# Kernel tuning notes

Measured on AMD Instinct MI355X. Metric: run time of the kernel, lower is better.

The kernel has to match this reference:

```python
import jax, jax.numpy as jnp
import numpy as np

N0, N1, N2 = 200000, 50000, 10000   # node counts per hop (src -> layer1 targets -> layer2 targets)
E1, E2 = 1000000, 250000
C_IN, H = 128, 256


def setup_inputs() -> dict:
    key = jax.random.key(0)
    ks = jax.random.split(key, 10)
    return {
        "x": jax.random.normal(ks[0], (N0, C_IN), dtype=jnp.float32),
        "src1": jax.random.randint(ks[1], (E1,), 0, N0, dtype=jnp.int32),
        "dst1": jax.random.randint(ks[2], (E1,), 0, N1, dtype=jnp.int32),
        "src2": jax.random.randint(ks[3], (E2,), 0, N1, dtype=jnp.int32),
        "dst2": jax.random.randint(ks[4], (E2,), 0, N2, dtype=jnp.int32),
        "Wl1": jax.random.normal(ks[5], (C_IN, H), dtype=jnp.float32) / np.sqrt(C_IN),
        "Wr1": jax.random.normal(ks[6], (C_IN, H), dtype=jnp.float32) / np.sqrt(C_IN),
        "b1": jnp.zeros((H,), dtype=jnp.float32),
        "Wl2": jax.random.normal(ks[7], (H, H), dtype=jnp.float32) / np.sqrt(H),
        "Wr2": jax.random.normal(ks[8], (H, H), dtype=jnp.float32) / np.sqrt(H),
        "b2": jnp.zeros((H,), dtype=jnp.float32),
    }


def _sage_conv(x_src, x_dst, src, dst, Wl, Wr, b, n_dst):
    # mean aggregation of neighbor messages (PyG SAGEConv, aggr='mean', root_weight=True)
    msgs = x_src[src]                                             # [E, C] irregular gather
    agg = jax.ops.segment_sum(msgs, dst, num_segments=n_dst)      # [n_dst, C]
    cnt = jax.ops.segment_sum(jnp.ones_like(dst, dtype=x_src.dtype), dst, num_segments=n_dst)
    agg = agg / jnp.maximum(cnt, 1.0)[:, None]
    return agg @ Wl + x_dst @ Wr + b


def reference(x, src1, dst1, src2, dst2, Wl1, Wr1, b1, Wl2, Wr2, b2):
    # layer 1: targets are first N1 nodes
    h = _sage_conv(x, x[:N1], src1, dst1, Wl1, Wr1, b1, N1)       # [N1, H]
    h = jax.nn.relu(h)                                            # dropout: eval mode (identity)
    # layer 2: targets are first N2 nodes of the layer-1 output
    out = _sage_conv(h, h[:N2], src2, dst2, Wl2, Wr2, b2, N2)     # [N2, H]
    return out
```

## Files before the change

kernel.cpp:

```cpp
#include <hip/hip_runtime.h>

#define N0 200000
#define N1 50000
#define N2 10000
#define E1 1000000
#define E2 250000
#define CIN 128
#define HD  256

#define SH1   6
#define PK1   18
#define NB1   782
#define CAP1  2048
#define DPB1  64
#define DPB1H 32
#define NB1L  1564
#define EB1H  1440
#define SH2   4
#define PK2   16
#define NB2   625
#define CAP2  640
#define DPB2  16

#define NBIN1 489
#define NBIN2 123
#define NPREP 768
#define NCVT  25000

#define EB2   (CAP2 + 128)

typedef __attribute__((ext_vector_type(8))) short short8;
typedef __attribute__((ext_vector_type(4))) float f32x4;
typedef __attribute__((ext_vector_type(2))) float f32x2;

__device__ __forceinline__ unsigned short f2bf(float f) {
    unsigned u = __builtin_bit_cast(unsigned, f);
    u = (u + 0x7fffu + ((u >> 16) & 1u)) >> 16;
    return (unsigned short)u;
}
__device__ __forceinline__ float bf2f(unsigned short h) {
    unsigned u = ((unsigned)h) << 16;
    return __builtin_bit_cast(float, u);
}

__device__ __forceinline__ unsigned enc_fp8x4(float a, float b, float c, float d) {
#if __has_builtin(__builtin_amdgcn_cvt_pk_fp8_f32)
    int p = 0;
    p = __builtin_amdgcn_cvt_pk_fp8_f32(a, b, p, false);
    p = __builtin_amdgcn_cvt_pk_fp8_f32(c, d, p, true);
    return (unsigned)p;
#else
    float vv[4] = {a, b, c, d};
    unsigned out = 0;
    #pragma unroll
    for (int k = 0; k < 4; k++) {
        float f = fminf(fmaxf(vv[k], -448.f), 448.f);
        unsigned u = __builtin_bit_cast(unsigned, f);
        const unsigned s = (u >> 24) & 0x80u;
        u &= 0x7fffffffu;
        unsigned byte;
        if (u < 0x3C800000u) {
            const float af = __builtin_bit_cast(float, u);
            byte = s | (unsigned)(int)rintf(af * 512.0f);
        } else {
            const unsigned u2 = u + 0x000FFFFFu + ((u >> 20) & 1u);
            const unsigned e  = (u2 >> 23) - 120u;
            byte = s | ((e & 0xFu) << 3) | ((u2 >> 20) & 7u);
        }
        out |= byte << (8 * k);
    }
    return out;
#endif
}

__device__ __forceinline__ unsigned char enc_fp8_1(float v) {
#if __has_builtin(__builtin_amdgcn_cvt_pk_fp8_f32)
    const int p = __builtin_amdgcn_cvt_pk_fp8_f32(v, v, 0, false);
    return (unsigned char)(p & 0xFF);
#else
    float f = fminf(fmaxf(v, -448.f), 448.f);
    unsigned u = __builtin_bit_cast(unsigned, f);
    const unsigned s = (u >> 24) & 0x80u;
    u &= 0x7fffffffu;
    unsigned byte;
    if (u < 0x3C800000u) {
        const float af = __builtin_bit_cast(float, u);
        byte = s | (unsigned)(int)rintf(af * 512.0f);
    } else {
        const unsigned u2 = u + 0x000FFFFFu + ((u >> 20) & 1u);
        const unsigned e  = (u2 >> 23) - 120u;
        byte = s | ((e & 0xFu) << 3) | ((u2 >> 20) & 7u);
    }
    return (unsigned char)byte;
#endif
}

__device__ __forceinline__ void acc_fp8x4(unsigned w, float* __restrict__ acc) {
#if __has_builtin(__builtin_amdgcn_cvt_pk_f32_fp8)
    const f32x2 lo = __builtin_amdgcn_cvt_pk_f32_fp8((int)w, false);
    const f32x2 hi = __builtin_amdgcn_cvt_pk_f32_fp8((int)w, true);
    acc[0] += lo[0]; acc[1] += lo[1]; acc[2] += hi[0]; acc[3] += hi[1];
#else
    #pragma unroll
    for (int k = 0; k < 4; k++) {
        const unsigned b8   = (w >> (8 * k)) & 0xFFu;
        const unsigned bits = ((b8 & 0x80u) << 24) | ((b8 & 0x7Fu) << 20);
        acc[k] += __builtin_bit_cast(float, bits) * 0x1p120f;
    }
#endif
}

template<int SHIFTB, int PACKSH, int CAP>
__device__ __forceinline__ void bin_body(
    int bb, const int* __restrict__ src, const int* __restrict__ dst,
    int* __restrict__ gcnt, unsigned* __restrict__ binned, int E, int* sh)
{
    int* hcnt  = sh;
    int* hbase = sh + 1024;
    int* hcur  = sh + 2048;
    const int t = threadIdx.x;
    #pragma unroll
    for (int j = 0; j < 4; j++) hcnt[t + j * 256] = 0;
    __syncthreads();

    unsigned pk[8];
    int      bk[8];
    const int e0 = bb * 2048;
    #pragma unroll
    for (int j = 0; j < 8; j++) {
        const int e = e0 + j * 256 + t;
        if (e < E) {
            const int d = dst[e];
            const int s = src[e];
            bk[j] = d >> SHIFTB;
            pk[j] = ((unsigned)(d & ((1 << SHIFTB) - 1)) << PACKSH) | (unsigned)s;
            atomicAdd(&hcnt[bk[j]], 1);
        } else bk[j] = -1;
    }
    __syncthreads();

    #pragma unroll
    for (int j = 0; j < 4; j++) {
        const int i = t + j * 256;
        hbase[i] = atomicAdd(&gcnt[i], hcnt[i]);
        hcur[i]  = 0;
    }
    __syncthreads();

    #pragma unroll
    for (int j = 0; j < 8; j++) {
        if (bk[j] >= 0) {
            const int idx = atomicAdd(&hcur[bk[j]], 1);
            binned[(size_t)bk[j] * CAP + hbase[bk[j]] + idx] = pk[j];
        }
    }
}

__global__ __launch_bounds__(256) void megaA_kernel(
    const float* __restrict__ x, unsigned short* __restrict__ xb,
    unsigned char* __restrict__ xf8, unsigned char* __restrict__ hb8,
    const float* __restrict__ Wl1, const float* __restrict__ Wr1,
    const float* __restrict__ Wl2, const float* __restrict__ Wr2,
    unsigned short* __restrict__ wsw1, unsigned short* __restrict__ wsw2,
    const int* __restrict__ src1, const int* __restrict__ dst1,
    const int* __restrict__ src2, const int* __restrict__ dst2,
    int* __restrict__ gcnt1, int* __restrict__ gcnt2,
    unsigned* __restrict__ binned1, unsigned* __restrict__ binned2)
{
    __shared__ int sh[3072];
    const int b = blockIdx.x;
    const int t = threadIdx.x;

    if (b < NBIN1) {
        bin_body<SH1, PK1, CAP1>(b, src1, dst1, gcnt1, binned1, E1, sh);
    } else if (b < NBIN1 + NBIN2) {
        bin_body<SH2, PK2, CAP2>(b - NBIN1, src2, dst2, gcnt2, binned2, E2, sh);
    } else if (b < NBIN1 + NBIN2 + NPREP) {
        const int pb = b - NBIN1 - NBIN2;
        const float* Wl; const float* Wr; unsigned short* wsw; int K, tid;
        if (pb < 256) { Wl = Wl1; Wr = Wr1; wsw = wsw1; K = CIN; tid = pb * 256 + t; }
        else          { Wl = Wl2; Wr = Wr2; wsw = wsw2; K = HD;  tid = (pb - 256) * 256 + t; }
        const int j  = tid & 7;
        const int L  = (tid >> 3) & 63;
        const int nt = (tid >> 9) & 15;
        const int kt = tid >> 13;
        const int k  = kt * 32 + (L >> 4) * 8 + j;
        const int n  = nt * 16 + (L & 15);
        const float v = (k < K) ? Wl[(size_t)k * HD + n]
                                : Wr[(size_t)(k - K) * HD + n];
        wsw[tid] = f2bf(v);
    } else if (b < NBIN1 + NBIN2 + NPREP + NCVT) {
        const int i = (b - NBIN1 - NBIN2 - NPREP) * 256 + t;
        const f32x4 v = __builtin_nontemporal_load(&((const f32x4*)x)[i]);
        ((unsigned*)xf8)[i] = enc_fp8x4(v.x, v.y, v.z, v.w);
        if (i < N1 * (CIN / 4)) {
            ushort4 o;
            o.x = f2bf(v.x); o.y = f2bf(v.y); o.z = f2bf(v.z); o.w = f2bf(v.w);
            ((ushort4*)xb)[i] = o;
        }
    } else {
        if (t < 32)  ((unsigned*)(xf8 + (size_t)N0 * CIN))[t] = 0u;
        if (t < 64)  ((unsigned*)(hb8 + (size_t)N1 * HD))[t] = 0u;
    }
}

__global__ __launch_bounds__(512) void layer1_mega(
    const unsigned short* __restrict__ xb, const unsigned char* __restrict__ xf8,
    const unsigned* __restrict__ binned1, const int* __restrict__ gcnt1,
    const unsigned short* __restrict__ wsw1, const float* __restrict__ bias,
    unsigned short* __restrict__ hb, unsigned char* __restrict__ hb8)
{
    __shared__ int ebuf[EB1H];
    __shared__ int lhist[DPB1H], loff[DPB1H], lcur[DPB1H];
    __shared__ __align__(16) unsigned short aggT[4 * DPB1H * 4 * 8];

    const int t = threadIdx.x;
    const int b = blockIdx.x;
    const int B = b >> 1;
    const int H = b & 1;
    const int cnt = gcnt1[B];
    const unsigned* bp = binned1 + (size_t)B * CAP1;

    if (t < DPB1H) lhist[t] = 0;
    __syncthreads();
    for (int i = t; i < cnt; i += 512) {
        const int r = (int)(bp[i] >> PK1) - H * DPB1H;
        if ((unsigned)r < (unsigned)DPB1H) atomicAdd(&lhist[r], 1);
    }
    __syncthreads();
    if (t < DPB1H) {
        const int p8 = (lhist[t] + 7) & ~7;
        int sum = p8;
        #pragma unroll
        for (int ofs = 1; ofs < DPB1H; ofs <<= 1) {
            const int u = __shfl_up(sum, ofs);
            if (t >= ofs) sum += u;
        }
        const int st = sum - p8;
        loff[t] = st; lcur[t] = st;
    }
    __syncthreads();
    for (int i = t; i < cnt; i += 512) {
        const unsigned p = bp[i];
        const int r = (int)(p >> PK1) - H * DPB1H;
        if ((unsigned)r < (unsigned)DPB1H) {
            const int slot = atomicAdd(&lcur[r], 1);
            ebuf[slot] = (int)(p & ((1u << PK1) - 1u));
        }
    }
    __syncthreads();
    if (t < DPB1H) {
        const int h = lhist[t];
        const int np = (h + 7) & ~7;
        const int s0 = loff[t];
        for (int i = s0 + h; i < s0 + np; i++) ebuf[i] = N0;
    }
    __syncthreads();

    const int w = t >> 6, L = t & 63;
    const int qd = L >> 4, l16 = L & 15;
    const unsigned char* xp8 = xf8 + (size_t)l16 * 8;
    {
        const int r = w * 4 + qd;
        const int base = loff[r];
        const int n    = lhist[r];
        const int npad = (n + 7) & ~7;
        float acc[8];
        #pragma unroll
        for (int j = 0; j < 8; j++) acc[j] = 0.f;
        for (int i = 0; i < npad; i += 8) {
            uint2 v[8];
            #pragma unroll
            for (int u = 0; u < 8; u++) {
                const int s = ebuf[base + i + u];
                v[u] = *(const uint2*)(xp8 + (size_t)s * CIN);
            }
            #pragma unroll
            for (int u = 0; u < 8; u++) {
                acc_fp8x4(v[u].x, acc);
                acc_fp8x4(v[u].y, acc + 4);
            }
        }
        const float sc = 1.0f / fmaxf((float)n, 1.0f);
        short8 o;
        #pragma unroll
        for (int j = 0; j < 8; j++) o[j] = (short)f2bf(acc[j] * sc);
        const int kt = l16 >> 2, q = l16 & 3;
        *(short8*)&aggT[((kt * DPB1H + r) * 4 + q) * 8] = o;
    }
    __syncthreads();

    const int m = L & 15, q = L >> 4;
    const int mt = w & 1, nq = w >> 1;
    const int row_l = mt * 16 + m;
    const int rg2 = min(b * DPB1H + row_l, N1 - 1);
    const unsigned short* a2p = xb + (size_t)rg2 * CIN + q * 8;

    f32x4 acc[4];
    #pragma unroll
    for (int nt = 0; nt < 4; nt++) acc[nt] = (f32x4){0.f, 0.f, 0.f, 0.f};

    #pragma unroll
    for (int kt = 0; kt < 8; kt++) {
        short8 af;
        if (kt < 4) af = *(const short8*)&aggT[((kt * DPB1H + row_l) * 4 + q) * 8];
        else        af = *(const short8*)(a2p + (kt - 4) * 32);
        #pragma unroll
        for (int nt = 0; nt < 4; nt++) {
            const int ntg = nq * 4 + nt;
            const short8 bf = *(const short8*)(
                wsw1 + (((size_t)kt * 16 + ntg) * 64 + L) * 8);
            acc[nt] = __builtin_amdgcn_mfma_f32_16x16x32_bf16(af, bf, acc[nt], 0, 0, 0);
        }
    }

    const int orow0 = b * DPB1H + mt * 16 + q * 4;
    #pragma unroll
    for (int nt = 0; nt < 4; nt++) {
        const int col = (nq * 4 + nt) * 16 + m;
        const float bv = bias[col];
        #pragma unroll
        for (int r = 0; r < 4; r++) {
            const int row = orow0 + r;
            if (row < N1) {
                const float v = fmaxf(acc[nt][r] + bv, 0.0f);
                hb8[(size_t)row * HD + col] = enc_fp8_1(v);
                if (row < N2) hb[(size_t)row * HD + col] = f2bf(v);
            }
        }
    }
}

__global__ __launch_bounds__(512) void layer2_mega(
    const unsigned short* __restrict__ hb, const unsigned char* __restrict__ hb8,
    const unsigned* __restrict__ binned2, const int* __restrict__ gcnt2,
    const unsigned short* __restrict__ wsw2, const float* __restrict__ bias,
    float* __restrict__ outp)
{
    __shared__ int ebuf[EB2];
    __shared__ int lhist[DPB2], loff[DPB2], lcur[DPB2];
    __shared__ __align__(16) unsigned short aggT[8 * DPB2 * 4 * 8];

    const int t = threadIdx.x;
    const int b = blockIdx.x;
    const int cnt = gcnt2[b];
    const unsigned* bp = binned2 + (size_t)b * CAP2;

    if (t < DPB2) lhist[t] = 0;
    __syncthreads();
    for (int i = t; i < cnt; i += 512)
        atomicAdd(&lhist[bp[i] >> PK2], 1);
    __syncthreads();
    if (t < DPB2) {
        const int p8 = (lhist[t] + 7) & ~7;
        int sum = p8;
        #pragma unroll
        for (int ofs = 1; ofs < DPB2; ofs <<= 1) {
            const int u = __shfl_up(sum, ofs);
            if (t >= ofs) sum += u;
        }
        const int st = sum - p8;
        loff[t] = st; lcur[t] = st;
    }
    __syncthreads();
    for (int i = t; i < cnt; i += 512) {
        const unsigned p = bp[i];
        const int slot = atomicAdd(&lcur[p >> PK2], 1);
        ebuf[slot] = (int)(p & 0xFFFFu);
    }
    __syncthreads();
    if (t < DPB2) {
        const int h = lhist[t];
        const int np = (h + 7) & ~7;
        const int s0 = loff[t];
        for (int i = s0 + h; i < s0 + np; i++) ebuf[i] = N1;
    }
    __syncthreads();

    const int w = t >> 6, L = t & 63;
    const int hf = L >> 5, l32 = L & 31;
    {
        const int r = w * 2 + hf;
        const int base = loff[r];
        const int n    = lhist[r];
        const int npad = (n + 7) & ~7;
        float acc[8];
        #pragma unroll
        for (int j = 0; j < 8; j++) acc[j] = 0.f;
        const unsigned char* hp8 = hb8 + (size_t)l32 * 8;
        for (int i = 0; i < npad; i += 8) {
            uint2 v[8];
            #pragma unroll
            for (int u = 0; u < 8; u++) {
                const int s = ebuf[base + i + u];
                v[u] = *(const uint2*)(hp8 + (size_t)s * HD);
            }
            #pragma unroll
            for (int u = 0; u < 8; u++) {
                acc_fp8x4(v[u].x, acc);
                acc_fp8x4(v[u].y, acc + 4);
            }
        }
        const float sc = 1.0f / fmaxf((float)n, 1.0f);
        short8 o;
        #pragma unroll
        for (int j = 0; j < 8; j++) o[j] = (short)f2bf(acc[j] * sc);
        const int kt = l32 >> 2, q = l32 & 3;
        *(short8*)&aggT[((kt * DPB2 + r) * 4 + q) * 8] = o;
    }
    __syncthreads();

    const int m = L & 15, q = L >> 4;
    const int rg2 = b * DPB2 + m;
    const unsigned short* a2p = hb + (size_t)rg2 * HD + q * 8;

    f32x4 acc[2];
    acc[0] = (f32x4){0.f, 0.f, 0.f, 0.f};
    acc[1] = (f32x4){0.f, 0.f, 0.f, 0.f};

    #pragma unroll
    for (int kt = 0; kt < 16; kt++) {
        short8 af;
        if (kt < 8) af = *(const short8*)&aggT[((kt * DPB2 + m) * 4 + q) * 8];
        else        af = *(const short8*)(a2p + (kt - 8) * 32);
        #pragma unroll
        for (int nt = 0; nt < 2; nt++) {
            const short8 bf = *(const short8*)(
                wsw2 + (((size_t)kt * 16 + (w * 2 + nt)) * 64 + L) * 8);
            acc[nt] = __builtin_amdgcn_mfma_f32_16x16x32_bf16(af, bf, acc[nt], 0, 0, 0);
        }
    }

    const int orow0 = b * DPB2 + q * 4;
    #pragma unroll
    for (int nt = 0; nt < 2; nt++) {
        const int col = (w * 2 + nt) * 16 + m;
        const float bv = bias[col];
        #pragma unroll
        for (int r = 0; r < 4; r++)
            outp[(size_t)(orow0 + r) * HD + col] = acc[nt][r] + bv;
    }
}

extern "C" void kernel_launch(void* const* d_in, const int* in_sizes, int n_in,
                              void* d_out, int out_size, void* d_ws, size_t ws_size,
                              hipStream_t stream)
{
    const float* x    = (const float*)d_in[0];
    const int*   src1 = (const int*)  d_in[1];
    const int*   dst1 = (const int*)  d_in[2];
    const int*   src2 = (const int*)  d_in[3];
    const int*   dst2 = (const int*)  d_in[4];
    const float* Wl1  = (const float*)d_in[5];
    const float* Wr1  = (const float*)d_in[6];
    const float* b1   = (const float*)d_in[7];
    const float* Wl2  = (const float*)d_in[8];
    const float* Wr2  = (const float*)d_in[9];
    const float* b2   = (const float*)d_in[10];
    float* out = (float*)d_out;

    unsigned short* xb   = (unsigned short*)d_ws;
    unsigned char*  xf8  = (unsigned char*)(xb + (size_t)N1 * CIN);
    unsigned short* hb   = (unsigned short*)(xf8 + (size_t)(N0 + 2) * CIN);
    unsigned char*  hb8  = (unsigned char*)(hb + (size_t)N2 * HD);
    unsigned short* wsw1 = (unsigned short*)(hb8 + (size_t)(N1 + 1) * HD + 256);
    unsigned short* wsw2 = wsw1 + 2 * CIN * HD;
    int* gcnt1 = (int*)(wsw2 + 2 * HD * HD);
    int* gcnt2 = gcnt1 + 1024;
    unsigned* binned1 = (unsigned*)(gcnt2 + 1024);
    unsigned* binned2 = binned1 + (size_t)NB1 * CAP1;

    hipMemsetAsync(gcnt1, 0, 2048 * sizeof(int), stream);

    megaA_kernel<<<NBIN1 + NBIN2 + NPREP + NCVT + 1, 256, 0, stream>>>(
        x, xb, xf8, hb8, Wl1, Wr1, Wl2, Wr2, wsw1, wsw2,
        src1, dst1, src2, dst2, gcnt1, gcnt2, binned1, binned2);

    layer1_mega<<<NB1L, 512, 0, stream>>>(xb, xf8, binned1, gcnt1, wsw1, b1, hb, hb8);
    layer2_mega<<<NB2, 512, 0, stream>>>(hb, hb8, binned2, gcnt2, wsw2, b2, out);
}
```

Measured before the change: 259.1 us.

## Split layer-2 blocks in half to double grid and per-row gather width

```diff
diff --git a/kernel.cpp b/kernel.cpp
--- a/kernel.cpp
+++ b/kernel.cpp
@@ -21,13 +21,14 @@
 #define NB2   625
 #define CAP2  640
 #define DPB2  16
+#define DPB2H 8
+#define NB2L  1250
+#define EB2H  704
 
 #define NBIN1 489
 #define NBIN2 123
 #define NPREP 768
 #define NCVT  25000
-
-#define EB2   (CAP2 + 128)
 
 typedef __attribute__((ext_vector_type(8))) short short8;
 typedef __attribute__((ext_vector_type(4))) float f32x4;
@@ -337,25 +338,29 @@
     const unsigned short* __restrict__ wsw2, const float* __restrict__ bias,
     float* __restrict__ outp)
 {
-    __shared__ int ebuf[EB2];
-    __shared__ int lhist[DPB2], loff[DPB2], lcur[DPB2];
-    __shared__ __align__(16) unsigned short aggT[8 * DPB2 * 4 * 8];
+    __shared__ int ebuf[EB2H];
+    __shared__ int lhist[DPB2H], loff[DPB2H], lcur[DPB2H];
+    __shared__ __align__(16) unsigned short aggT[8 * DPB2H * 4 * 8];
 
     const int t = threadIdx.x;
     const int b = blockIdx.x;
-    const int cnt = gcnt2[b];
-    const unsigned* bp = binned2 + (size_t)b * CAP2;
-
-    if (t < DPB2) lhist[t] = 0;
-    __syncthreads();
-    for (int i = t; i < cnt; i += 512)
-        atomicAdd(&lhist[bp[i] >> PK2], 1);
-    __syncthreads();
-    if (t < DPB2) {
+    const int B = b >> 1;
+    const int H = b & 1;
+    const int cnt = gcnt2[B];
+    const unsigned* bp = binned2 + (size_t)B * CAP2;
+
+    if (t < DPB2H) lhist[t] = 0;
+    __syncthreads();
+    for (int i = t; i < cnt; i += 512) {
+        const int r = (int)(bp[i] >> PK2) - H * DPB2H;
+        if ((unsigned)r < (unsigned)DPB2H) atomicAdd(&lhist[r], 1);
+    }
+    __syncthreads();
+    if (t < DPB2H) {
         const int p8 = (lhist[t] + 7) & ~7;
         int sum = p8;
         #pragma unroll
-        for (int ofs = 1; ofs < DPB2; ofs <<= 1) {
+        for (int ofs = 1; ofs < DPB2H; ofs <<= 1) {
             const int u = __shfl_up(sum, ofs);
             if (t >= ofs) sum += u;
         }
@@ -365,11 +370,14 @@
     __syncthreads();
     for (int i = t; i < cnt; i += 512) {
         const unsigned p = bp[i];
-        const int slot = atomicAdd(&lcur[p >> PK2], 1);
-        ebuf[slot] = (int)(p & 0xFFFFu);
-    }
-    __syncthreads();
-    if (t < DPB2) {
+        const int r = (int)(p >> PK2) - H * DPB2H;
+        if ((unsigned)r < (unsigned)DPB2H) {
+            const int slot = atomicAdd(&lcur[r], 1);
+            ebuf[slot] = (int)(p & 0xFFFFu);
+        }
+    }
+    __syncthreads();
+    if (t < DPB2H) {
         const int h = lhist[t];
         const int np = (h + 7) & ~7;
         const int s0 = loff[t];
@@ -378,40 +386,37 @@
     __syncthreads();
 
     const int w = t >> 6, L = t & 63;
-    const int hf = L >> 5, l32 = L & 31;
     {
-        const int r = w * 2 + hf;
+        const int r = w;
         const int base = loff[r];
         const int n    = lhist[r];
         const int npad = (n + 7) & ~7;
-        float acc[8];
-        #pragma unroll
-        for (int j = 0; j < 8; j++) acc[j] = 0.f;
-        const unsigned char* hp8 = hb8 + (size_t)l32 * 8;
+        float acc[4];
+        #pragma unroll
+        for (int j = 0; j < 4; j++) acc[j] = 0.f;
+        const unsigned char* hp8 = hb8 + (size_t)L * 4;
         for (int i = 0; i < npad; i += 8) {
-            uint2 v[8];
+            unsigned v[8];
             #pragma unroll
             for (int u = 0; u < 8; u++) {
                 const int s = ebuf[base + i + u];
-                v[u] = *(const uint2*)(hp8 + (size_t)s * HD);
+                v[u] = *(const unsigned*)(hp8 + (size_t)s * HD);
             }
             #pragma unroll
-            for (int u = 0; u < 8; u++) {
-                acc_fp8x4(v[u].x, acc);
-                acc_fp8x4(v[u].y, acc + 4);
-            }
+            for (int u = 0; u < 8; u++) acc_fp8x4(v[u], acc);
         }
         const float sc = 1.0f / fmaxf((float)n, 1.0f);
-        short8 o;
-        #pragma unroll
-        for (int j = 0; j < 8; j++) o[j] = (short)f2bf(acc[j] * sc);
-        const int kt = l32 >> 2, q = l32 & 3;
-        *(short8*)&aggT[((kt * DPB2 + r) * 4 + q) * 8] = o;
+        ushort4 o;
+        o.x = f2bf(acc[0] * sc); o.y = f2bf(acc[1] * sc);
+        o.z = f2bf(acc[2] * sc); o.w = f2bf(acc[3] * sc);
+        const int kt = L >> 3, q = (L >> 1) & 3, jo = (L & 1) * 4;
+        *(ushort4*)&aggT[(((kt * DPB2H + r) * 4 + q) * 8) + jo] = o;
     }
     __syncthreads();
 
     const int m = L & 15, q = L >> 4;
-    const int rg2 = b * DPB2 + m;
+    const int m8 = m & 7;
+    const int rg2 = b * DPB2H + m8;
     const unsigned short* a2p = hb + (size_t)rg2 * HD + q * 8;
 
     f32x4 acc[2];
@@ -421,7 +426,7 @@
     #pragma unroll
     for (int kt = 0; kt < 16; kt++) {
         short8 af;
-        if (kt < 8) af = *(const short8*)&aggT[((kt * DPB2 + m) * 4 + q) * 8];
+        if (kt < 8) af = *(const short8*)&aggT[((kt * DPB2H + m8) * 4 + q) * 8];
         else        af = *(const short8*)(a2p + (kt - 8) * 32);
         #pragma unroll
         for (int nt = 0; nt < 2; nt++) {
@@ -431,14 +436,16 @@
         }
     }
 
-    const int orow0 = b * DPB2 + q * 4;
-    #pragma unroll
-    for (int nt = 0; nt < 2; nt++) {
-        const int col = (w * 2 + nt) * 16 + m;
-        const float bv = bias[col];
-        #pragma unroll
-        for (int r = 0; r < 4; r++)
-            outp[(size_t)(orow0 + r) * HD + col] = acc[nt][r] + bv;
+    if (q < 2) {
+        const int orow0 = b * DPB2H + q * 4;
+        #pragma unroll
+        for (int nt = 0; nt < 2; nt++) {
+            const int col = (w * 2 + nt) * 16 + m;
+            const float bv = bias[col];
+            #pragma unroll
+            for (int r = 0; r < 4; r++)
+                outp[(size_t)(orow0 + r) * HD + col] = acc[nt][r] + bv;
+        }
     }
 }
 
@@ -477,5 +484,5 @@
         src1, dst1, src2, dst2, gcnt1, gcnt2, binned1, binned2);
 
     layer1_mega<<<NB1L, 512, 0, stream>>>(xb, xf8, binned1, gcnt1, wsw1, b1, hb, hb8);
-    layer2_mega<<<NB2, 512, 0, stream>>>(hb, hb8, binned2, gcnt2, wsw2, b2, out);
-}
+    layer2_mega<<<NB2L, 512, 0, stream>>>(hb, hb8, binned2, gcnt2, wsw2, b2, out);
+}
```

Result: slower. 266.5 us (+2.8%).
